# Optimization experiments

Measured on AMD Instinct MI355X. Metric: run time of the kernel, lower is better.

Reference implementation:

```python
import jax, jax.numpy as jnp
import numpy as np

N = 4096      # num_nodes (tokens)
D = 1024      # in_features
GC1 = 1024    # gc hidden sizes
GC2 = 1024
FC1 = 512     # fc hidden
NUM_CLASSES = 2
FW = 8        # forward band width
BW = 8        # backward band width


def setup_inputs() -> dict:
    key = jax.random.key(0)
    ks = jax.random.split(key, 6)
    s = 0.02
    return {
        "x": jax.random.normal(ks[0], (N, D), jnp.float32),
        # sequential band weights, initialized to 0.5 as in the module
        "fw_w": 0.5 * jnp.ones((FW,), jnp.float32),
        "bw_w": 0.5 * jnp.ones((BW,), jnp.float32),
        # graph-conv layer weights (linear: h @ W + b, then A @ .)
        "gc_w1": s * jax.random.normal(ks[1], (D, GC1), jnp.float32),
        "gc_b1": jnp.zeros((GC1,), jnp.float32),
        "gc_w2": s * jax.random.normal(ks[2], (GC1, GC2), jnp.float32),
        "gc_b2": jnp.zeros((GC2,), jnp.float32),
        # fully-connected head
        "fc_w1": s * jax.random.normal(ks[3], (GC2, FC1), jnp.float32),
        "fc_b1": jnp.zeros((FC1,), jnp.float32),
        "fc_w2": s * jax.random.normal(ks[4], (FC1, NUM_CLASSES), jnp.float32),
        "fc_b2": jnp.zeros((NUM_CLASSES,), jnp.float32),
    }


def build_adjacency(fw_w, bw_w, n):
    # banded adjacency: self-loops + forward superdiagonals + backward subdiagonals,
    # then symmetric normalization D^{-1/2} A D^{-1/2}
    a = jnp.eye(n, dtype=fw_w.dtype)
    for j in range(fw_w.shape[0]):          # small fixed band loop (FW)
        a = a + fw_w[j] * jnp.eye(n, k=j + 1, dtype=fw_w.dtype)
    for j in range(bw_w.shape[0]):          # small fixed band loop (BW)
        a = a + bw_w[j] * jnp.eye(n, k=-(j + 1), dtype=bw_w.dtype)
    d = a.sum(axis=1) ** -0.5               # row degrees
    return d[:, None] * a * d[None, :]


def reference(x, fw_w, bw_w, gc_w1, gc_b1, gc_w2, gc_b2, fc_w1, fc_b1, fc_w2, fc_b2):
    a = build_adjacency(fw_w, bw_w, x.shape[0])          # [N, N]
    # GC layers: selu(A @ (H W + b)); dropout=0.0 -> identity
    h = jax.nn.selu(a @ (x @ gc_w1 + gc_b1))             # [N, GC1]
    h = jax.nn.selu(a @ (h @ gc_w2 + gc_b2))             # [N, GC2]
    pooled = h.mean(axis=0)                              # mean pooling over nodes
    z = jax.nn.selu(pooled @ fc_w1 + fc_b1)              # [FC1]
    return z @ fc_w2 + fc_b2                             # [NUM_CLASSES] logits
```

## Files before the change

### kernel.cpp

```cpp
#include <hip/hip_runtime.h>
#include <stdint.h>

#define NND 4096
#define DIM 1024
#define FC1N 512

typedef __attribute__((ext_vector_type(8))) short short8;
typedef __attribute__((ext_vector_type(4))) float floatx4;
typedef unsigned short u16;
typedef unsigned int u32;

__device__ __forceinline__ u16 f2bf(float f) {
    union { float f; u32 u; } a; a.f = f;
    u32 u = a.u;
    return (u16)((u + 0x7fffu + ((u >> 16) & 1u)) >> 16);
}
__device__ __forceinline__ float bf2f(u16 h) {
    union { u32 u; float f; } a; a.u = ((u32)h) << 16; return a.f;
}
__device__ __forceinline__ float selu_f(float x) {
    const float lam = 1.0507009873554805f;
    const float alp = 1.6732632423543772f;
    return x > 0.f ? lam * x : lam * alp * (expf(x) - 1.f);
}
__device__ __forceinline__ void async16(const u16* g, u16* l) {
    __builtin_amdgcn_global_load_lds((const __attribute__((address_space(1))) u32*)g,
                                     (__attribute__((address_space(3))) u32*)l, 16, 0, 0);
}
__device__ __forceinline__ float dinv_row(int i, const float* fw, const float* bw) {
    if (i < 0 || i >= NND) return 0.f;
    float deg = 1.f;
    #pragma unroll
    for (int j = 0; j < 8; ++j) {
        if (i + j + 1 < NND) deg += fw[j];
        if (i - j - 1 >= 0)  deg += bw[j];
    }
    return 1.f / sqrtf(deg);
}

__global__ void k_prep(const float* __restrict__ x, const float* __restrict__ w1,
                       const float* __restrict__ w2, const float* __restrict__ fw,
                       const float* __restrict__ bw, u16* __restrict__ XA,
                       u16* __restrict__ W1t, u16* __restrict__ W2t,
                       float* __restrict__ fzone) {
    __shared__ __align__(16) char smem[32768];
    int b = blockIdx.x, t = threadIdx.x;
    if (b < 1024) {
        __shared__ float sdv_s[32];
        __shared__ float wts_s[17];
        int m0 = (b >> 2) * 16;
        int c0 = (b & 3) * 256;
        if (t < 32) sdv_s[t] = dinv_row(m0 - 8 + t, fw, bw);
        else if (t >= 64 && t < 81) {
            int o = t - 72;
            wts_s[t - 64] = (o == 0) ? 1.f : (o > 0 ? fw[o - 1] : bw[-o - 1]);
        }
        float (*tile)[256] = (float(*)[256])smem;
        int row = t >> 3, seg = t & 7;
        int g = m0 - 8 + row;
        g = g < 0 ? 0 : (g > NND - 1 ? NND - 1 : g);
        const float4* src = (const float4*)x + (size_t)g * 256 + (c0 >> 2);
        float4* trow = (float4*)tile[row];
        #pragma unroll
        for (int i = 0; i < 8; ++i) trow[seg + i * 8] = src[seg + i * 8];
        __syncthreads();
        float w[17];
        #pragma unroll
        for (int o = 0; o < 17; ++o) w[o] = wts_s[o];
        float win[17];
        #pragma unroll
        for (int j = 0; j < 16; ++j) win[j] = sdv_s[j] * tile[j][t];
        #pragma unroll
        for (int rr = 0; rr < 16; ++rr) {
            win[(rr + 16) % 17] = sdv_s[rr + 16] * tile[rr + 16][t];
            float a = 0.f;
            #pragma unroll
            for (int o = 0; o < 17; ++o) a += w[o] * win[(rr + o) % 17];
            XA[(size_t)(m0 + rr) * DIM + c0 + t] = f2bf(a * sdv_s[8 + rr]);
        }
        return;
    }
    if (b == 1536) {
        for (int i = t; i < 1537; i += 256) fzone[i] = 0.f;
        return;
    }
    if (b >= 1537) {
        float* rs = fzone + 2048;
        float fwr[8], bwr[8];
        #pragma unroll
        for (int j = 0; j < 8; ++j) { fwr[j] = fw[j]; bwr[j] = bw[j]; }
        float* dv = (float*)smem;
        int i0 = (b - 1537) * 256;
        #pragma unroll
        for (int half = 0; half < 2; ++half) {
            int idx = t + half * 256;
            if (idx < 272) {
                int i = i0 - 8 + idx;
                float dvv = 0.f;
                if (i >= 0 && i < NND) {
                    float deg = 1.f;
                    #pragma unroll
                    for (int j = 0; j < 8; ++j) {
                        if (i + j + 1 < NND) deg += fwr[j];
                        if (i - j - 1 >= 0)  deg += bwr[j];
                    }
                    dvv = 1.f / sqrtf(deg);
                }
                dv[idx] = dvv;
            }
        }
        __syncthreads();
        float di = dv[t + 8];
        float s = di;
        #pragma unroll
        for (int k = 1; k <= 8; ++k)
            s += fwr[k - 1] * dv[t + 8 + k] + bwr[k - 1] * dv[t + 8 - k];
        rs[i0 + t] = di * s;
        return;
    }
    int job = b - 1024;
    const float* in = (job & 256) ? w2 : w1;
    u16* out = (job & 256) ? W2t : W1t;
    int tl = job & 255;
    int r0 = (tl >> 4) * 64, c0 = (tl & 15) * 64;
    float (*tile)[65] = (float(*)[65])smem;
    int cg = t & 15, rb = t >> 4;
    #pragma unroll
    for (int rr = 0; rr < 4; ++rr) {
        int row = rb + rr * 16;
        float4 v = *(const float4*)(in + (size_t)(r0 + row) * DIM + c0 + cg * 4);
        tile[row][cg * 4 + 0] = v.x; tile[row][cg * 4 + 1] = v.y;
        tile[row][cg * 4 + 2] = v.z; tile[row][cg * 4 + 3] = v.w;
    }
    __syncthreads();
    #pragma unroll
    for (int rr = 0; rr < 4; ++rr) {
        int nl = rb + rr * 16;
        int kl = cg * 4;
        ushort4 o;
        o.x = f2bf(tile[kl + 0][nl]); o.y = f2bf(tile[kl + 1][nl]);
        o.z = f2bf(tile[kl + 2][nl]); o.w = f2bf(tile[kl + 3][nl]);
        *(ushort4*)(out + (size_t)(c0 + nl) * DIM + r0 + kl) = o;
    }
}

__global__ void k_band(const u16* __restrict__ in, u16* __restrict__ outp,
                       const float* __restrict__ fw, const float* __restrict__ bw) {
    __shared__ __align__(16) u16 tile[32][256];
    __shared__ float sdv_s[32];
    __shared__ float wts_s[17];
    int b = blockIdx.x, t = threadIdx.x;
    int m0 = (b >> 2) * 16;
    int c0 = (b & 3) * 256;
    if (t < 32) sdv_s[t] = dinv_row(m0 - 8 + t, fw, bw);
    else if (t >= 64 && t < 81) {
        int o = t - 72;
        wts_s[t - 64] = (o == 0) ? 1.f : (o > 0 ? fw[o - 1] : bw[-o - 1]);
    }
    int row = t >> 3, seg = t & 7;
    int g = m0 - 8 + row;
    g = g < 0 ? 0 : (g > NND - 1 ? NND - 1 : g);
    const uint4* src = (const uint4*)(in + (size_t)g * DIM + c0);
    uint4* trow = (uint4*)tile[row];
    #pragma unroll
    for (int i = 0; i < 4; ++i) trow[seg + i * 8] = src[seg + i * 8];
    __syncthreads();
    float w[17];
    #pragma unroll
    for (int o = 0; o < 17; ++o) w[o] = wts_s[o];
    float win[17];
    #pragma unroll
    for (int j = 0; j < 16; ++j) win[j] = sdv_s[j] * bf2f(tile[j][t]);
    #pragma unroll
    for (int rr = 0; rr < 16; ++rr) {
        win[(rr + 16) % 17] = sdv_s[rr + 16] * bf2f(tile[rr + 16][t]);
        float a = 0.f;
        #pragma unroll
        for (int o = 0; o < 17; ++o) a += w[o] * win[(rr + o) % 17];
        outp[(size_t)(m0 + rr) * DIM + c0 + t] = f2bf(a * sdv_s[8 + rr]);
    }
}

__launch_bounds__(256, 1)
__global__ void k_gemm(const u16* __restrict__ A, const u16* __restrict__ Bt,
                       const float* __restrict__ bias, const float* __restrict__ rs,
                       u16* __restrict__ H, float* __restrict__ pooled, int mode) {
    __shared__ __align__(16) u16 stage[2][16384];
    const int m0 = blockIdx.x * 128, n0 = blockIdx.y * 128;
    const int t = threadIdx.x, wave = t >> 6, lane = t & 63;
    const int q = lane >> 4, r = lane & 15;
    const int wm = wave & 1, wn = wave >> 1;
    const int Lrow = lane >> 3, Lseg = lane & 7;

    floatx4 acc[4][4];
    #pragma unroll
    for (int i = 0; i < 4; ++i)
        #pragma unroll
        for (int j = 0; j < 4; ++j) acc[i][j] = (floatx4)0.f;

    #pragma unroll
    for (int i = 0; i < 8; ++i) {
        int c = wave * 8 + i;
        u16* dst = &stage[0][c * 512];
        const u16* src = (c < 16)
            ? A  + (size_t)(m0 + c * 8 + Lrow) * DIM + ((Lseg ^ Lrow) * 8)
            : Bt + (size_t)(n0 + (c - 16) * 8 + Lrow) * DIM + ((Lseg ^ Lrow) * 8);
        async16(src, dst);
    }

    #pragma unroll 1
    for (int k = 0; k < 16; ++k) {
        int cur = k & 1;
        __syncthreads();
        if (k < 15) {
            int kb = (k + 1) * 64;
            #pragma unroll
            for (int i = 0; i < 8; ++i) {
                int c = wave * 8 + i;
                u16* dst = &stage[cur ^ 1][c * 512];
                const u16* src = (c < 16)
                    ? A  + (size_t)(m0 + c * 8 + Lrow) * DIM + kb + ((Lseg ^ Lrow) * 8)
                    : Bt + (size_t)(n0 + (c - 16) * 8 + Lrow) * DIM + kb + ((Lseg ^ Lrow) * 8);
                async16(src, dst);
            }
        }
        const u16* As = &stage[cur][0];
        const u16* Bs = &stage[cur][8192];
        #pragma unroll
        for (int s = 0; s < 2; ++s) {
            int j0 = s * 4 + q;
            short8 bfr[4];
            #pragma unroll
            for (int nt = 0; nt < 4; ++nt) {
                int nl = wn * 64 + nt * 16 + r;
                bfr[nt] = *(const short8*)&Bs[nl * 64 + ((j0 ^ (nl & 7)) * 8)];
            }
            #pragma unroll
            for (int mt = 0; mt < 4; ++mt) {
                int ml = wm * 64 + mt * 16 + r;
                short8 afr = *(const short8*)&As[ml * 64 + ((j0 ^ (ml & 7)) * 8)];
                #pragma unroll
                for (int nt = 0; nt < 4; ++nt)
                    acc[mt][nt] = __builtin_amdgcn_mfma_f32_16x16x32_bf16(afr, bfr[nt], acc[mt][nt], 0, 0, 0);
            }
        }
    }

    float psum[4] = {0.f, 0.f, 0.f, 0.f};
    float bv[4];
    #pragma unroll
    for (int nt = 0; nt < 4; ++nt) bv[nt] = bias[n0 + wn * 64 + nt * 16 + r];
    #pragma unroll
    for (int mt = 0; mt < 4; ++mt) {
        #pragma unroll
        for (int rr = 0; rr < 4; ++rr) {
            int m = m0 + wm * 64 + mt * 16 + q * 4 + rr;
            float rsm = rs[m];
            #pragma unroll
            for (int nt = 0; nt < 4; ++nt) {
                float v = selu_f(acc[mt][nt][rr] + rsm * bv[nt]);
                if (mode == 0)
                    H[(size_t)m * DIM + n0 + wn * 64 + nt * 16 + r] = f2bf(v);
                else psum[nt] += v;
            }
        }
    }
    if (mode) {
        float* PL = (float*)&stage[0][0];
        #pragma unroll
        for (int nt = 0; nt < 4; ++nt)
            PL[(wn * 64 + nt * 16 + r) * 8 + wm * 4 + q] = psum[nt];
        __syncthreads();
        if (t < 128) {
            float s = 0.f;
            #pragma unroll
            for (int i = 0; i < 8; ++i) s += PL[t * 8 + i];
            atomicAdd(&pooled[n0 + t], s);
        }
    }
}

__global__ void k_fc(const float* __restrict__ pooled, const float* __restrict__ fcw1,
                     const float* __restrict__ fcb1, const float* __restrict__ fcw2,
                     const float* __restrict__ fcb2, float* __restrict__ zacc,
                     u32* __restrict__ cnt, float* __restrict__ out) {
    __shared__ float red[1024];
    __shared__ int lastf;
    int o = threadIdx.x, b = blockIdx.x;
    int kb = b * 64;
    float s = 0.f;
    #pragma unroll 4
    for (int kk = 0; kk < 64; ++kk)
        s += pooled[kb + kk] * fcw1[(size_t)(kb + kk) * FC1N + o];
    atomicAdd(&zacc[o], s * (1.f / NND));
    __threadfence();
    __syncthreads();
    if (o == 0) lastf = (atomicAdd(cnt, 1u) == 15u);
    __syncthreads();
    if (!lastf) return;
    __threadfence();
    float zv = atomicAdd(&zacc[o], 0.f);
    float z = selu_f(zv + fcb1[o]);
    red[o] = z * fcw2[o * 2 + 0];
    red[512 + o] = z * fcw2[o * 2 + 1];
    __syncthreads();
    #pragma unroll 1
    for (int s2 = 256; s2 > 0; s2 >>= 1) {
        if (o < s2) { red[o] += red[o + s2]; red[512 + o] += red[512 + o + s2]; }
        __syncthreads();
    }
    if (o == 0) { out[0] = red[0] + fcb2[0]; out[1] = red[1] + fcb2[1]; }
}

extern "C" void kernel_launch(void* const* d_in, const int* in_sizes, int n_in,
                              void* d_out, int out_size, void* d_ws, size_t ws_size,
                              hipStream_t stream) {
    const float* x     = (const float*)d_in[0];
    const float* fw    = (const float*)d_in[1];
    const float* bw    = (const float*)d_in[2];
    const float* gc_w1 = (const float*)d_in[3];
    const float* gc_b1 = (const float*)d_in[4];
    const float* gc_w2 = (const float*)d_in[5];
    const float* gc_b2 = (const float*)d_in[6];
    const float* fc_w1 = (const float*)d_in[7];
    const float* fc_b1 = (const float*)d_in[8];
    const float* fc_w2 = (const float*)d_in[9];
    const float* fc_b2 = (const float*)d_in[10];
    float* out = (float*)d_out;

    char* ws = (char*)d_ws;
    u16*   XA     = (u16*)(ws);
    u16*   H1     = (u16*)(ws + (8u  << 20));
    u16*   H1A    = (u16*)(ws + (16u << 20));
    u16*   W1t    = (u16*)(ws + (24u << 20));
    u16*   W2t    = (u16*)(ws + (26u << 20));
    float* fzone  = (float*)(ws + (28u << 20));
    float* pooled = fzone;
    float* zacc   = fzone + 1024;
    u32*   cnt    = (u32*)(fzone + 1536);
    float* rs     = fzone + 2048;

    k_prep<<<1553, 256, 0, stream>>>(x, gc_w1, gc_w2, fw, bw, XA, W1t, W2t, fzone);
    k_gemm<<<dim3(32, 8), 256, 0, stream>>>(XA, W1t, gc_b1, rs, H1, nullptr, 0);
    k_band<<<1024, 256, 0, stream>>>(H1, H1A, fw, bw);
    k_gemm<<<dim3(32, 8), 256, 0, stream>>>(H1A, W2t, gc_b2, rs, nullptr, pooled, 1);
    k_fc<<<16, 512, 0, stream>>>(pooled, fc_w1, fc_b1, fc_w2, fc_b2, zacc, cnt, out);
}
```

Measured before the change: 153.3 us.

## Triple-buffer GEMM LDS staging with explicit waitcnt and priority scheduling

Replaces the double-buffered async global-to-LDS pipeline in the bf16 MFMA GEMM with a three-stage ring that keeps two tiles in flight. It uses explicit vmcnt waits, raw s_barrier and sched_barrier instead of __syncthreads. It also raises wave priority with s_setprio during the MFMA section. The aim is to hide global memory latency better and cut barrier stalls. In exchange the kernel uses 96KB of LDS per block, and the code now depends on hand-counted vmcnt values matching the number of async loads per stage.

After: 160.9 us. +5.0%, slower.

```diff
diff --git a/kernel.cpp b/kernel.cpp
--- a/kernel.cpp
+++ b/kernel.cpp
@@ -185,7 +185,7 @@
 __global__ void k_gemm(const u16* __restrict__ A, const u16* __restrict__ Bt,
                        const float* __restrict__ bias, const float* __restrict__ rs,
                        u16* __restrict__ H, float* __restrict__ pooled, int mode) {
-    __shared__ __align__(16) u16 stage[2][16384];
+    __shared__ __align__(16) u16 stage[3][16384];
     const int m0 = blockIdx.x * 128, n0 = blockIdx.y * 128;
     const int t = threadIdx.x, wave = t >> 6, lane = t & 63;
     const int q = lane >> 4, r = lane & 15;
@@ -198,34 +198,21 @@
         #pragma unroll
         for (int j = 0; j < 4; ++j) acc[i][j] = (floatx4)0.f;
 
-    #pragma unroll
-    for (int i = 0; i < 8; ++i) {
-        int c = wave * 8 + i;
-        u16* dst = &stage[0][c * 512];
-        const u16* src = (c < 16)
-            ? A  + (size_t)(m0 + c * 8 + Lrow) * DIM + ((Lseg ^ Lrow) * 8)
-            : Bt + (size_t)(n0 + (c - 16) * 8 + Lrow) * DIM + ((Lseg ^ Lrow) * 8);
-        async16(src, dst);
-    }
-
-    #pragma unroll 1
-    for (int k = 0; k < 16; ++k) {
-        int cur = k & 1;
-        __syncthreads();
-        if (k < 15) {
-            int kb = (k + 1) * 64;
-            #pragma unroll
-            for (int i = 0; i < 8; ++i) {
-                int c = wave * 8 + i;
-                u16* dst = &stage[cur ^ 1][c * 512];
-                const u16* src = (c < 16)
-                    ? A  + (size_t)(m0 + c * 8 + Lrow) * DIM + kb + ((Lseg ^ Lrow) * 8)
-                    : Bt + (size_t)(n0 + (c - 16) * 8 + Lrow) * DIM + kb + ((Lseg ^ Lrow) * 8);
-                async16(src, dst);
-            }
-        }
-        const u16* As = &stage[cur][0];
-        const u16* Bs = &stage[cur][8192];
+    auto STAGE = [&](int kt, int buf) {
+        int kb = kt * 64;
+        #pragma unroll
+        for (int i = 0; i < 8; ++i) {
+            int c = wave * 8 + i;
+            u16* dst = &stage[buf][c * 512];
+            const u16* src = (c < 16)
+                ? A  + (size_t)(m0 + c * 8 + Lrow) * DIM + kb + ((Lseg ^ Lrow) * 8)
+                : Bt + (size_t)(n0 + (c - 16) * 8 + Lrow) * DIM + kb + ((Lseg ^ Lrow) * 8);
+            async16(src, dst);
+        }
+    };
+    auto COMPUTE = [&](int buf) {
+        const u16* As = &stage[buf][0];
+        const u16* Bs = &stage[buf][8192];
         #pragma unroll
         for (int s = 0; s < 2; ++s) {
             int j0 = s * 4 + q;
@@ -244,7 +231,31 @@
                     acc[mt][nt] = __builtin_amdgcn_mfma_f32_16x16x32_bf16(afr, bfr[nt], acc[mt][nt], 0, 0, 0);
             }
         }
-    }
+    };
+
+    STAGE(0, 0); STAGE(1, 1); STAGE(2, 2);
+
+    #pragma unroll 1
+    for (int k = 0; k < 14; ++k) {
+        asm volatile("s_waitcnt vmcnt(16)" ::: "memory");
+        __builtin_amdgcn_s_barrier();
+        __builtin_amdgcn_sched_barrier(0);
+        __builtin_amdgcn_s_setprio(1);
+        COMPUTE(k % 3);
+        __builtin_amdgcn_s_setprio(0);
+        asm volatile("s_waitcnt lgkmcnt(0)" ::: "memory");
+        __builtin_amdgcn_s_barrier();
+        __builtin_amdgcn_sched_barrier(0);
+        if (k < 13) STAGE(k + 3, k % 3);
+    }
+    asm volatile("s_waitcnt vmcnt(8)" ::: "memory");
+    __builtin_amdgcn_s_barrier();
+    __builtin_amdgcn_sched_barrier(0);
+    COMPUTE(2);
+    asm volatile("s_waitcnt vmcnt(0)" ::: "memory");
+    __builtin_amdgcn_s_barrier();
+    __builtin_amdgcn_sched_barrier(0);
+    COMPUTE(0);
 
     float psum[4] = {0.f, 0.f, 0.f, 0.f};
     float bv[4];
@@ -266,7 +277,7 @@
         }
     }
     if (mode) {
-        float* PL = (float*)&stage[0][0];
+        float* PL = (float*)&stage[1][0];
         #pragma unroll
         for (int nt = 0; nt < 4; ++nt)
             PL[(wn * 64 + nt * 16 + r) * 8 + wm * 4 + q] = psum[nt];
```
